# Kernel tuning notes

Hardware: AMD Instinct MI355X
Metric: run time of the kernel (lower is better)

## Reference

```python
import jax, jax.numpy as jnp
import numpy as np

DIM = 768
NUM_HEADS = 12
HEAD_DIM = 64  # attn_head_dim override
ALL_HEAD_DIM = NUM_HEADS * HEAD_DIM  # 768
SCALE = HEAD_DIM ** -0.5


def setup_inputs() -> dict:
    key = jax.random.key(0)
    ks = jax.random.split(key, 6)
    B, N = 8, 1024
    x = jax.random.normal(ks[0], (B, N, DIM), dtype=jnp.float32)
    w_qkv = jax.random.normal(ks[1], (3 * ALL_HEAD_DIM, DIM), dtype=jnp.float32) * (DIM ** -0.5)
    q_bias = jnp.zeros((ALL_HEAD_DIM,), dtype=jnp.float32)
    v_bias = jnp.zeros((ALL_HEAD_DIM,), dtype=jnp.float32)
    w_proj = jax.random.normal(ks[2], (DIM, ALL_HEAD_DIM), dtype=jnp.float32) * (ALL_HEAD_DIM ** -0.5)
    b_proj = jnp.zeros((DIM,), dtype=jnp.float32)
    return {"x": x, "w_qkv": w_qkv, "q_bias": q_bias, "v_bias": v_bias,
            "w_proj": w_proj, "b_proj": b_proj}


def reference(x, w_qkv, q_bias, v_bias, w_proj, b_proj):
    B, N, C = x.shape
    # qkv bias: [q_bias, zeros (k has no bias), v_bias]
    qkv_bias = jnp.concatenate([q_bias, jnp.zeros_like(v_bias), v_bias])
    qkv = x @ w_qkv.T + qkv_bias                      # [B, N, 3*ALL_HEAD_DIM]
    qkv = qkv.reshape(B, N, 3, NUM_HEADS, HEAD_DIM).transpose(2, 0, 3, 1, 4)
    q, k, v = qkv[0], qkv[1], qkv[2]                  # each [B, H, N, D]
    attn = jnp.einsum('bhqd,bhkd->bhqk', q * SCALE, k)
    attn = jax.nn.softmax(attn, axis=-1)
    out = jnp.einsum('bhqk,bhkd->bhqd', attn, v)      # [B, H, N, D]
    out = out.transpose(0, 2, 1, 3).reshape(B, N, ALL_HEAD_DIM)
    out = out @ w_proj.T + b_proj                     # [B, N, C]
    return out
```

## Files before the change

kernel.cpp:

```cpp
#include <hip/hip_runtime.h>
#include <hip/hip_bf16.h>

typedef unsigned short u16;
typedef unsigned int u32;
typedef __attribute__((ext_vector_type(4))) float f32x4;
typedef __attribute__((ext_vector_type(16))) float f32x16;
typedef __attribute__((ext_vector_type(8))) short bf16x8;

__device__ inline u16 f2bf(float f) {
    union { float f; u32 u; } v; v.f = f;
    u32 r = v.u + 0x7fff + ((v.u >> 16) & 1);
    return (u16)(r >> 16);
}

__device__ inline f32x4 mfma16(bf16x8 a, bf16x8 b, f32x4 c) {
    return __builtin_amdgcn_mfma_f32_16x16x32_bf16(a, b, c, 0, 0, 0);
}
__device__ inline f32x16 mfma32(bf16x8 a, bf16x8 b, f32x16 c) {
    return __builtin_amdgcn_mfma_f32_32x32x16_bf16(a, b, c, 0, 0, 0);
}
__device__ inline u32 cvtpk(float lo, float hi) {
    u32 r;
    asm("v_cvt_pk_bf16_f32 %0, %1, %2" : "=v"(r) : "v"(lo), "v"(hi));
    return r;
}
__device__ inline float exp2v(float x) {
    float r;
    asm("v_exp_f32 %0, %1" : "=v"(r) : "v"(x));
    return r;
}

__device__ inline void gload_lds16(const void* g, const void* l) {
    __builtin_amdgcn_global_load_lds(
        (const __attribute__((address_space(1))) void*)g,
        (__attribute__((address_space(3))) void*)l, 16, 0, 0);
}

#define QSCALE 0.18033688f

__global__ void cvt_kernel(const float* __restrict__ in, u16* __restrict__ out, int n8) {
    int i = blockIdx.x * 256 + threadIdx.x;
    if (i >= n8) return;
    const float4* p = (const float4*)in;
    float4 a = p[2 * i], b = p[2 * i + 1];
    bf16x8 v;
    v[0] = (short)f2bf(a.x); v[1] = (short)f2bf(a.y);
    v[2] = (short)f2bf(a.z); v[3] = (short)f2bf(a.w);
    v[4] = (short)f2bf(b.x); v[5] = (short)f2bf(b.y);
    v[6] = (short)f2bf(b.z); v[7] = (short)f2bf(b.w);
    ((bf16x8*)out)[i] = v;
}

template <int EPI>
__global__ __launch_bounds__(256) void gemm_bt(
    const u16* __restrict__ A, const u16* __restrict__ B,
    int M, int N, int K,
    u16* __restrict__ qw, u16* __restrict__ kw, u16* __restrict__ vw,
    const float* __restrict__ qb, const float* __restrict__ vb,
    float* __restrict__ outp, const float* __restrict__ bproj)
{
    __shared__ __align__(16) u16 smem[16384];
    u16* lA0 = smem;
    u16* lA1 = smem + 4096;
    u16* lB0 = smem + 8192;
    u16* lB1 = smem + 12288;

    const int tid = threadIdx.x;
    const int lane = tid & 63;
    const int wv = tid >> 6;
    const int nbn = N >> 7;
    const int nwg = gridDim.x;
    const int wg = (blockIdx.x & 7) * (nwg >> 3) + (blockIdx.x >> 3);
    const int bm = wg / nbn, bn = wg % nbn;
    const int row0 = bm << 7, col0 = bn << 7;

    const int c0 = tid, c1 = tid + 256;
    const int ldsOff0 = (wv * 64) * 8;
    const int ldsOff1 = (256 + wv * 64) * 8;

    f32x4 acc[4][4];
#pragma unroll
    for (int i = 0; i < 4; i++)
#pragma unroll
        for (int j = 0; j < 4; j++) acc[i][j] = (f32x4){0.f, 0.f, 0.f, 0.f};

    const int nT = K >> 5;

    auto stage = [&](u16* bufA, u16* bufB, int t) {
        const int k0 = t << 5;
        gload_lds16(&A[(size_t)(row0 + (c0 >> 2)) * K + k0 + (c0 & 3) * 8], bufA + ldsOff0);
        gload_lds16(&A[(size_t)(row0 + (c1 >> 2)) * K + k0 + (c1 & 3) * 8], bufA + ldsOff1);
        gload_lds16(&B[(size_t)(col0 + (c0 >> 2)) * K + k0 + (c0 & 3) * 8], bufB + ldsOff0);
        gload_lds16(&B[(size_t)(col0 + (c1 >> 2)) * K + k0 + (c1 & 3) * 8], bufB + ldsOff1);
    };

    const int wr = (wv >> 1) << 6;
    const int wc = (wv & 1) << 6;

    stage(lA0, lB0, 0);
    __syncthreads();
    for (int t = 0; t < nT; ++t) {
        const u16* As = ((t & 1) ? lA1 : lA0) + (wr + (lane & 15)) * 32 + ((lane >> 4) * 8);
        const u16* Bs = ((t & 1) ? lB1 : lB0) + (wc + (lane & 15)) * 32 + ((lane >> 4) * 8);
        if (t + 1 < nT)
            stage((t & 1) ? lA0 : lA1, (t & 1) ? lB0 : lB1, t + 1);
        bf16x8 af[4], bfr[4];
#pragma unroll
        for (int i = 0; i < 4; i++) af[i] = *(const bf16x8*)(As + i * 16 * 32);
#pragma unroll
        for (int i = 0; i < 4; i++) bfr[i] = *(const bf16x8*)(Bs + i * 16 * 32);
#pragma unroll
        for (int i = 0; i < 4; i++)
#pragma unroll
            for (int j = 0; j < 4; j++)
                acc[i][j] = mfma16(af[i], bfr[j], acc[i][j]);
        __syncthreads();
    }

    if (EPI == 0) {
        const int part = col0 / 768;
        const int colr0 = col0 - part * 768;
        const int h0 = colr0 >> 6;
        const int bb = row0 >> 10;
        const int n0 = row0 & 1023;

        if (part < 2) {
#pragma unroll
            for (int nj = 0; nj < 4; ++nj) {
                const int col = wc + nj * 16 + (lane & 15);
                const float bias = (part == 0) ? qb[colr0 + col] : 0.f;
                const float sc = (part == 0) ? QSCALE : 1.f;
#pragma unroll
                for (int mi = 0; mi < 4; ++mi) {
#pragma unroll
                    for (int j = 0; j < 4; ++j) {
                        const int row = wr + mi * 16 + ((lane >> 4) << 2) + j;
                        smem[row * 128 + ((((col >> 3) ^ (row & 7)) << 3) | (col & 7))] =
                            f2bf((acc[mi][nj][j] + bias) * sc);
                    }
                }
            }
        } else {
#pragma unroll
            for (int nj = 0; nj < 4; ++nj) {
                const int col = wc + nj * 16 + (lane & 15);
                const float bias = vb[colr0 + col];
#pragma unroll
                for (int mi = 0; mi < 4; ++mi) {
                    const int row = wr + mi * 16 + ((lane >> 4) << 2);
                    ushort4 pk;
                    pk.x = f2bf(acc[mi][nj][0] + bias);
                    pk.y = f2bf(acc[mi][nj][1] + bias);
                    pk.z = f2bf(acc[mi][nj][2] + bias);
                    pk.w = f2bf(acc[mi][nj][3] + bias);
                    *(ushort4*)&smem[col * 128 +
                        ((((row >> 3) ^ (col & 7)) << 3) | (row & 7))] = pk;
                }
            }
        }
        __syncthreads();

        if (part == 0) {
#pragma unroll
            for (int p = 0; p < 8; ++p) {
                const int c = p * 256 + tid;
                const int h = c >> 10, ri = (c >> 3) & 127, j = c & 7;
                bf16x8 v = *(const bf16x8*)&smem[ri * 128 + (((h * 8 + j) ^ (ri & 7)) << 3)];
                *(bf16x8*)&qw[((size_t)(((bb * 12 + h0 + h) << 10) + n0 + ri)) * 64 + j * 8] = v;
            }
        } else if (part == 1) {
#pragma unroll
            for (int p = 0; p < 8; ++p) {
                const int c = p * 256 + tid;
                const int h = c >> 10, t2 = (c >> 8) & 3, j = (c >> 5) & 7, r = c & 31;
                const int ri = t2 * 32 + r;
                bf16x8 v = *(const bf16x8*)&smem[ri * 128 + (((h * 8 + j) ^ (ri & 7)) << 3)];
                *(bf16x8*)&kw[((size_t)(bb * 12 + h0 + h) << 16) +
                              (((n0 >> 5) + t2) << 11) + (j << 8) + (r << 3)] = v;
            }
        } else {
#pragma unroll
            for (int p = 0; p < 8; ++p) {
                const int c = p * 256 + tid;
                const int h = c >> 10, w = c & 1023;
                const int t2 = w >> 8, f = (w >> 6) & 3, ln = w & 63;
                const int d = ((f >> 1) << 5) + (ln & 31);
                const int rb = t2 * 32 + ((f & 1) << 4) + ((ln >> 5) << 3);
                const int ct = h * 64 + d;
                bf16x8 v = *(const bf16x8*)&smem[ct * 128 + (((rb >> 3) ^ (ct & 7)) << 3)];
                *(bf16x8*)&vw[((size_t)(bb * 12 + h0 + h) << 16) +
                              (((n0 >> 5) + t2) << 11) + (f << 9) + (ln << 3)] = v;
            }
        }
    } else {
#pragma unroll
        for (int nj = 0; nj < 4; ++nj) {
            const int col = col0 + wc + nj * 16 + (lane & 15);
            const float bias = bproj[col];
#pragma unroll
            for (int mi = 0; mi < 4; ++mi) {
#pragma unroll
                for (int j = 0; j < 4; ++j) {
                    const int row = row0 + wr + mi * 16 + ((lane >> 4) << 2) + j;
                    outp[(size_t)row * N + col] = acc[mi][nj][j] + bias;
                }
            }
        }
    }
}

__global__ __launch_bounds__(256, 3) void attn_fwd(
    const u16* __restrict__ Q, const u16* __restrict__ KF,
    const u16* __restrict__ VF, u16* __restrict__ O)
{
    __shared__ __align__(16) u16 tlds[4][32 * 68];
    const int tid = threadIdx.x, lane = tid & 63, wv = tid >> 6;
    const int l31 = lane & 31, hi = lane >> 5;
    const int bh = blockIdx.x % 96;
    const int qbk = blockIdx.x / 96;
    const int q0 = qbk * 128 + wv * 32;
    const size_t base = (size_t)bh << 16;
    const u16* Qp = Q + base;
    const u16* Kp = KF + base;
    const u16* Vp = VF + base;

    bf16x8 qf0, qf1, qf2, qf3;
    {
        const u16* qrow = &Qp[(q0 + l31) * 64 + hi * 8];
        qf0 = *(const bf16x8*)(qrow);
        qf1 = *(const bf16x8*)(qrow + 16);
        qf2 = *(const bf16x8*)(qrow + 32);
        qf3 = *(const bf16x8*)(qrow + 48);
    }

    f32x16 ot0, ot1;
#pragma unroll
    for (int i = 0; i < 16; ++i) { ot0[i] = 0.f; ot1[i] = 0.f; }
    float m = -1e30f, l = 0.f;

    auto loadK = [&](int t2048, bf16x8& f0, bf16x8& f1, bf16x8& f2, bf16x8& f3) {
        const u16* kr = &Kp[t2048 + hi * 256 + l31 * 8];
        f0 = *(const bf16x8*)(kr);
        f1 = *(const bf16x8*)(kr + 512);
        f2 = *(const bf16x8*)(kr + 1024);
        f3 = *(const bf16x8*)(kr + 1536);
    };

    auto body = [&](int t2048, bf16x8 k0, bf16x8 k1, bf16x8 k2, bf16x8 k3) {
        f32x16 s;
#pragma unroll
        for (int i = 0; i < 16; ++i) s[i] = 0.f;
        __builtin_amdgcn_s_setprio(1);
        s = mfma32(k0, qf0, s);
        s = mfma32(k1, qf1, s);
        s = mfma32(k2, qf2, s);
        s = mfma32(k3, qf3, s);
        __builtin_amdgcn_s_setprio(0);
        const u16* vrow = &Vp[t2048 + lane * 8];
        bf16x8 vf00 = *(const bf16x8*)(vrow);
        bf16x8 vf01 = *(const bf16x8*)(vrow + 512);
        bf16x8 vf10 = *(const bf16x8*)(vrow + 1024);
        bf16x8 vf11 = *(const bf16x8*)(vrow + 1536);
        float t0 = fmaxf(fmaxf(s[0], s[1]), fmaxf(s[2], s[3]));
        float t1 = fmaxf(fmaxf(s[4], s[5]), fmaxf(s[6], s[7]));
        float t2 = fmaxf(fmaxf(s[8], s[9]), fmaxf(s[10], s[11]));
        float t3 = fmaxf(fmaxf(s[12], s[13]), fmaxf(s[14], s[15]));
        float tmax = fmaxf(fmaxf(t0, t1), fmaxf(t2, t3));
        tmax = fmaxf(tmax, __shfl_xor(tmax, 32));
        if (!__all(tmax - m <= 8.f)) {
            const float nm = fmaxf(m, tmax);
            const float cr = exp2v(m - nm);
#pragma unroll
            for (int i = 0; i < 16; ++i) { ot0[i] *= cr; ot1[i] *= cr; }
            l *= cr; m = nm;
        }
#pragma unroll
        for (int i = 0; i < 16; ++i) { float p = exp2v(s[i] - m); s[i] = p; l += p; }
        u32 w0 = cvtpk(s[0],  s[1]),  w1 = cvtpk(s[2],  s[3]);
        u32 w2 = cvtpk(s[4],  s[5]),  w3 = cvtpk(s[6],  s[7]);
        u32 w4 = cvtpk(s[8],  s[9]),  w5 = cvtpk(s[10], s[11]);
        u32 w6 = cvtpk(s[12], s[13]), w7 = cvtpk(s[14], s[15]);
        asm("v_permlane32_swap_b32 %0, %1" : "+v"(w0), "+v"(w2));
        asm("v_permlane32_swap_b32 %0, %1" : "+v"(w1), "+v"(w3));
        asm("v_permlane32_swap_b32 %0, %1" : "+v"(w4), "+v"(w6));
        asm("v_permlane32_swap_b32 %0, %1" : "+v"(w5), "+v"(w7));
        union { u32 u[4]; bf16x8 v; } pb0, pb1;
        pb0.u[0] = w0; pb0.u[1] = w1; pb0.u[2] = w2; pb0.u[3] = w3;
        pb1.u[0] = w4; pb1.u[1] = w5; pb1.u[2] = w6; pb1.u[3] = w7;
        __builtin_amdgcn_s_setprio(1);
        ot0 = mfma32(vf00, pb0.v, ot0);
        ot0 = mfma32(vf01, pb1.v, ot0);
        ot1 = mfma32(vf10, pb0.v, ot1);
        ot1 = mfma32(vf11, pb1.v, ot1);
        __builtin_amdgcn_s_setprio(0);
    };

    bf16x8 ka0, ka1, ka2, ka3, kb0, kb1, kb2, kb3;
    loadK(0, ka0, ka1, ka2, ka3);
    for (int kt = 0; kt < 32; kt += 2) {
        loadK((kt + 1) << 11, kb0, kb1, kb2, kb3);
        body(kt << 11, ka0, ka1, ka2, ka3);
        if (kt + 2 < 32) loadK((kt + 2) << 11, ka0, ka1, ka2, ka3);
        body((kt + 1) << 11, kb0, kb1, kb2, kb3);
    }

    const float lt = l + __shfl_xor(l, 32);
    const float inv = 1.f / lt;
    u16* tw = &tlds[wv][0];
    u32* tw32 = (u32*)tw;
#pragma unroll
    for (int i = 0; i < 8; ++i) {
        const int dl = 2 * (i & 1) + 8 * (i >> 1) + 4 * hi;
        tw32[(l31 * 68 + dl) >> 1]      = cvtpk(ot0[2 * i] * inv, ot0[2 * i + 1] * inv);
        tw32[(l31 * 68 + dl + 32) >> 1] = cvtpk(ot1[2 * i] * inv, ot1[2 * i + 1] * inv);
    }
    __syncthreads();
    const int b = bh / 12, h = bh - b * 12;
    const size_t obase = ((size_t)(b << 10) + q0) * 768 + h * 64 + (lane & 7) * 8;
#pragma unroll
    for (int it = 0; it < 4; ++it) {
        const int r = it * 8 + (lane >> 3);
        bf16x8 v = *(const bf16x8*)&tw[r * 68 + (lane & 7) * 8];
        *(bf16x8*)&O[obase + (size_t)r * 768] = v;
    }
}

extern "C" void kernel_launch(void* const* d_in, const int* in_sizes, int n_in,
                              void* d_out, int out_size, void* d_ws, size_t ws_size,
                              hipStream_t stream) {
    const float* x      = (const float*)d_in[0];
    const float* w_qkv  = (const float*)d_in[1];
    const float* q_bias = (const float*)d_in[2];
    const float* v_bias = (const float*)d_in[3];
    const float* w_proj = (const float*)d_in[4];
    const float* b_proj = (const float*)d_in[5];
    float* out = (float*)d_out;

    char* ws = (char*)d_ws;
    u16* xb     = (u16*)(ws);
    u16* wqkvb  = (u16*)(ws + 12582912);
    u16* wprojb = (u16*)(ws + 16121856);
    u16* qw     = (u16*)(ws + 17301504);
    u16* kw     = (u16*)(ws + 29884416);
    u16* vt     = (u16*)(ws + 42467328);
    u16* ob     = (u16*)(ws + 55050240);

    cvt_kernel<<<786432 / 256, 256, 0, stream>>>(x, xb, 786432);
    cvt_kernel<<<221184 / 256, 256, 0, stream>>>(w_qkv, wqkvb, 221184);
    cvt_kernel<<< 73728 / 256, 256, 0, stream>>>(w_proj, wprojb, 73728);

    gemm_bt<0><<<(8192 / 128) * (2304 / 128), 256, 0, stream>>>(
        xb, wqkvb, 8192, 2304, 768, qw, kw, vt, q_bias, v_bias, nullptr, nullptr);

    attn_fwd<<<96 * 8, 256, 0, stream>>>(qw, kw, vt, ob);

    gemm_bt<1><<<(8192 / 128) * (768 / 128), 256, 0, stream>>>(
        ob, wprojb, 8192, 768, 768, nullptr, nullptr, nullptr, nullptr, nullptr, out, b_proj);
}
```

Baseline: 123.3 us.

## Rewrite QKV GEMM with 256x256 tiles, 8 waves and triple-buffered LDS pipeline

Replaces the templated 128x128 QKV GEMM with a dedicated kernel that uses 256x256 tiles, 512 threads and a three-stage LDS ring with a swizzled layout. Each wave computes a 128x64 sub-tile, and MFMA priority hints are set around the inner products. The epilogue writes out the two 128-row halves in turn through shared memory. The aim is to raise data reuse per loaded byte and to hide global load latency, at the cost of 96KB of LDS per block, more registers, and only 288 blocks.

```diff
diff --git a/kernel.cpp b/kernel.cpp
--- a/kernel.cpp
+++ b/kernel.cpp
@@ -51,13 +51,188 @@
     ((bf16x8*)out)[i] = v;
 }
 
-template <int EPI>
-__global__ __launch_bounds__(256) void gemm_bt(
+__global__ __launch_bounds__(512, 2) void gemm_qkv(
     const u16* __restrict__ A, const u16* __restrict__ B,
-    int M, int N, int K,
     u16* __restrict__ qw, u16* __restrict__ kw, u16* __restrict__ vw,
-    const float* __restrict__ qb, const float* __restrict__ vb,
-    float* __restrict__ outp, const float* __restrict__ bproj)
+    const float* __restrict__ qb, const float* __restrict__ vb)
+{
+    __shared__ __align__(16) u16 smem[49152];
+    const int K = 768;
+    const int NT = 24;
+    const int tid = threadIdx.x;
+    const int lane = tid & 63, wv = tid >> 6;
+    const int wm = wv >> 2, wn = wv & 3;
+    const int wg = (blockIdx.x & 7) * 36 + (blockIdx.x >> 3);
+    const int bm = wg / 9, bn = wg % 9;
+    const int row0 = bm << 8, col0 = bn << 8;
+
+    const int srow = tid >> 2;
+    const int sch = (tid & 3) ^ ((srow >> 1) & 3);
+    const u16* gA = A + (size_t)(row0 + srow) * K + sch * 8;
+    const u16* gB = B + (size_t)(col0 + srow) * K + sch * 8;
+    const int ldst = wv * 512;
+
+    auto stageTile = [&](int bufi, int t) {
+        u16* base = &smem[bufi * 16384];
+        const int k0 = t << 5;
+        gload_lds16(gA + k0,                     base + ldst);
+        gload_lds16(gA + (size_t)128 * K + k0,   base + 4096 + ldst);
+        gload_lds16(gB + k0,                     base + 8192 + ldst);
+        gload_lds16(gB + (size_t)128 * K + k0,   base + 12288 + ldst);
+    };
+
+    const int arl = lane & 15, ahi = lane >> 4;
+    auto loadFrags = [&](int bufi, bf16x8 (&fa)[8], bf16x8 (&fb)[4]) {
+        const u16* bA = &smem[bufi * 16384 + wm * 4096];
+        const u16* bB = &smem[bufi * 16384 + 8192 + (wn >> 1) * 4096];
+#pragma unroll
+        for (int fi = 0; fi < 8; ++fi) {
+            const int rl = fi * 16 + arl;
+            const int chc = ahi ^ ((rl >> 1) & 3);
+            fa[fi] = *(const bf16x8*)(bA + rl * 32 + chc * 8);
+        }
+#pragma unroll
+        for (int fj = 0; fj < 4; ++fj) {
+            const int cl = ((wn & 1) << 6) + fj * 16 + arl;
+            const int chc = ahi ^ ((cl >> 1) & 3);
+            fb[fj] = *(const bf16x8*)(bB + cl * 32 + chc * 8);
+        }
+    };
+
+    f32x4 acc[8][4];
+#pragma unroll
+    for (int i = 0; i < 8; ++i)
+#pragma unroll
+        for (int j = 0; j < 4; ++j) acc[i][j] = (f32x4){0.f, 0.f, 0.f, 0.f};
+
+    auto mfmaTile = [&](bf16x8 (&fa)[8], bf16x8 (&fb)[4]) {
+#pragma unroll
+        for (int fi = 0; fi < 8; ++fi) {
+            __builtin_amdgcn_s_setprio(1);
+#pragma unroll
+            for (int fj = 0; fj < 4; ++fj)
+                acc[fi][fj] = mfma16(fa[fi], fb[fj], acc[fi][fj]);
+            __builtin_amdgcn_s_setprio(0);
+        }
+    };
+
+    bf16x8 ra[8], rb[4], sa[8], sb[4];
+
+    stageTile(0, 0); stageTile(1, 1); stageTile(2, 2);
+    asm volatile("s_waitcnt vmcnt(8)" ::: "memory");
+    __builtin_amdgcn_s_barrier();
+    loadFrags(0, ra, rb);
+    asm volatile("s_waitcnt lgkmcnt(0)" ::: "memory");
+    __builtin_amdgcn_sched_barrier(0);
+
+#pragma unroll 1
+    for (int t = 0; t < NT - 2; t += 2) {
+        asm volatile("s_waitcnt vmcnt(4)" ::: "memory");
+        __builtin_amdgcn_s_barrier();
+        stageTile(t % 3, t + 3);
+        loadFrags((t + 1) % 3, sa, sb);
+        mfmaTile(ra, rb);
+        asm volatile("s_waitcnt lgkmcnt(0)" ::: "memory");
+        __builtin_amdgcn_sched_barrier(0);
+        asm volatile("s_waitcnt vmcnt(4)" ::: "memory");
+        __builtin_amdgcn_s_barrier();
+        if (t + 4 < NT) stageTile((t + 1) % 3, t + 4);
+        loadFrags((t + 2) % 3, ra, rb);
+        mfmaTile(sa, sb);
+        asm volatile("s_waitcnt lgkmcnt(0)" ::: "memory");
+        __builtin_amdgcn_sched_barrier(0);
+    }
+    asm volatile("s_waitcnt vmcnt(0)" ::: "memory");
+    __builtin_amdgcn_s_barrier();
+    loadFrags((NT - 1) % 3, sa, sb);
+    mfmaTile(ra, rb);
+    mfmaTile(sa, sb);
+    __syncthreads();
+
+    const int part = col0 / 768;
+    const int colr0 = col0 - part * 768;
+    const int h0 = colr0 >> 6;
+
+#pragma unroll 1
+    for (int H = 0; H < 2; ++H) {
+        if (wm == H) {
+            if (part < 2) {
+#pragma unroll
+                for (int fj = 0; fj < 4; ++fj) {
+                    const int cl = wn * 64 + fj * 16 + arl;
+                    const float bias = (part == 0) ? qb[colr0 + cl] : 0.f;
+                    const float sc = (part == 0) ? QSCALE : 1.f;
+#pragma unroll
+                    for (int fi = 0; fi < 8; ++fi) {
+#pragma unroll
+                        for (int j = 0; j < 4; ++j) {
+                            const int rl = fi * 16 + (ahi << 2) + j;
+                            smem[rl * 256 + ((((cl >> 3) ^ (rl & 7)) << 3) | (cl & 7))] =
+                                f2bf((acc[fi][fj][j] + bias) * sc);
+                        }
+                    }
+                }
+            } else {
+#pragma unroll
+                for (int fj = 0; fj < 4; ++fj) {
+                    const int cl = wn * 64 + fj * 16 + arl;
+                    const float bias = vb[colr0 + cl];
+#pragma unroll
+                    for (int fi = 0; fi < 8; ++fi) {
+                        const int rl0 = fi * 16 + (ahi << 2);
+                        ushort4 pk;
+                        pk.x = f2bf(acc[fi][fj][0] + bias);
+                        pk.y = f2bf(acc[fi][fj][1] + bias);
+                        pk.z = f2bf(acc[fi][fj][2] + bias);
+                        pk.w = f2bf(acc[fi][fj][3] + bias);
+                        *(ushort4*)&smem[cl * 128 +
+                            ((((rl0 >> 3) ^ (cl & 7)) << 3) | (rl0 & 7))] = pk;
+                    }
+                }
+            }
+        }
+        __syncthreads();
+        const int bbH = (row0 + H * 128) >> 10;
+        const int n0H = (row0 + H * 128) & 1023;
+        if (part == 0) {
+#pragma unroll
+            for (int p = 0; p < 8; ++p) {
+                const int c = p * 512 + tid;
+                const int h = c >> 10, ri = (c >> 3) & 127, j = c & 7;
+                bf16x8 v = *(const bf16x8*)&smem[ri * 256 + ((((h << 3) + j) ^ (ri & 7)) << 3)];
+                *(bf16x8*)&qw[((size_t)(((bbH * 12 + h0 + h) << 10) + n0H + ri)) * 64 + j * 8] = v;
+            }
+        } else if (part == 1) {
+#pragma unroll
+            for (int p = 0; p < 8; ++p) {
+                const int c = p * 512 + tid;
+                const int h = c >> 10, t2 = (c >> 8) & 3, j = (c >> 5) & 7, r = c & 31;
+                const int ri = t2 * 32 + r;
+                bf16x8 v = *(const bf16x8*)&smem[ri * 256 + ((((h << 3) + j) ^ (ri & 7)) << 3)];
+                *(bf16x8*)&kw[((size_t)(bbH * 12 + h0 + h) << 16) +
+                              (((n0H >> 5) + t2) << 11) + (j << 8) + (r << 3)] = v;
+            }
+        } else {
+#pragma unroll
+            for (int p = 0; p < 8; ++p) {
+                const int c = p * 512 + tid;
+                const int h = c >> 10, w = c & 1023;
+                const int t2 = w >> 8, f = (w >> 6) & 3, ln = w & 63;
+                const int d = ((f >> 1) << 5) + (ln & 31);
+                const int rb_ = t2 * 32 + ((f & 1) << 4) + ((ln >> 5) << 3);
+                const int ct = h * 64 + d;
+                bf16x8 v = *(const bf16x8*)&smem[ct * 128 + (((rb_ >> 3) ^ (ct & 7)) << 3)];
+                *(bf16x8*)&vw[((size_t)(bbH * 12 + h0 + h) << 16) +
+                              (((n0H >> 5) + t2) << 11) + (f << 9) + (ln << 3)] = v;
+            }
+        }
+        __syncthreads();
+    }
+}
+
+__global__ __launch_bounds__(256) void gemm_proj(
+    const u16* __restrict__ A, const u16* __restrict__ B,
+    int M, int N, int K, float* __restrict__ outp, const float* __restrict__ bproj)
 {
     __shared__ __align__(16) u16 smem[16384];
     u16* lA0 = smem;
@@ -117,93 +292,16 @@
         __syncthreads();
     }
 
-    if (EPI == 0) {
-        const int part = col0 / 768;
-        const int colr0 = col0 - part * 768;
-        const int h0 = colr0 >> 6;
-        const int bb = row0 >> 10;
-        const int n0 = row0 & 1023;
-
-        if (part < 2) {
-#pragma unroll
-            for (int nj = 0; nj < 4; ++nj) {
-                const int col = wc + nj * 16 + (lane & 15);
-                const float bias = (part == 0) ? qb[colr0 + col] : 0.f;
-                const float sc = (part == 0) ? QSCALE : 1.f;
-#pragma unroll
-                for (int mi = 0; mi < 4; ++mi) {
-#pragma unroll
-                    for (int j = 0; j < 4; ++j) {
-                        const int row = wr + mi * 16 + ((lane >> 4) << 2) + j;
-                        smem[row * 128 + ((((col >> 3) ^ (row & 7)) << 3) | (col & 7))] =
-                            f2bf((acc[mi][nj][j] + bias) * sc);
-                    }
-                }
-            }
-        } else {
-#pragma unroll
-            for (int nj = 0; nj < 4; ++nj) {
-                const int col = wc + nj * 16 + (lane & 15);
-                const float bias = vb[colr0 + col];
-#pragma unroll
-                for (int mi = 0; mi < 4; ++mi) {
-                    const int row = wr + mi * 16 + ((lane >> 4) << 2);
-                    ushort4 pk;
-                    pk.x = f2bf(acc[mi][nj][0] + bias);
-                    pk.y = f2bf(acc[mi][nj][1] + bias);
-                    pk.z = f2bf(acc[mi][nj][2] + bias);
-                    pk.w = f2bf(acc[mi][nj][3] + bias);
-                    *(ushort4*)&smem[col * 128 +
-                        ((((row >> 3) ^ (col & 7)) << 3) | (row & 7))] = pk;
-                }
-            }
-        }
-        __syncthreads();
-
-        if (part == 0) {
-#pragma unroll
-            for (int p = 0; p < 8; ++p) {
-                const int c = p * 256 + tid;
-                const int h = c >> 10, ri = (c >> 3) & 127, j = c & 7;
-                bf16x8 v = *(const bf16x8*)&smem[ri * 128 + (((h * 8 + j) ^ (ri & 7)) << 3)];
-                *(bf16x8*)&qw[((size_t)(((bb * 12 + h0 + h) << 10) + n0 + ri)) * 64 + j * 8] = v;
-            }
-        } else if (part == 1) {
-#pragma unroll
-            for (int p = 0; p < 8; ++p) {
-                const int c = p * 256 + tid;
-                const int h = c >> 10, t2 = (c >> 8) & 3, j = (c >> 5) & 7, r = c & 31;
-                const int ri = t2 * 32 + r;
-                bf16x8 v = *(const bf16x8*)&smem[ri * 128 + (((h * 8 + j) ^ (ri & 7)) << 3)];
-                *(bf16x8*)&kw[((size_t)(bb * 12 + h0 + h) << 16) +
-                              (((n0 >> 5) + t2) << 11) + (j << 8) + (r << 3)] = v;
-            }
-        } else {
-#pragma unroll
-            for (int p = 0; p < 8; ++p) {
-                const int c = p * 256 + tid;
-                const int h = c >> 10, w = c & 1023;
-                const int t2 = w >> 8, f = (w >> 6) & 3, ln = w & 63;
-                const int d = ((f >> 1) << 5) + (ln & 31);
-                const int rb = t2 * 32 + ((f & 1) << 4) + ((ln >> 5) << 3);
-                const int ct = h * 64 + d;
-                bf16x8 v = *(const bf16x8*)&smem[ct * 128 + (((rb >> 3) ^ (ct & 7)) << 3)];
-                *(bf16x8*)&vw[((size_t)(bb * 12 + h0 + h) << 16) +
-                              (((n0 >> 5) + t2) << 11) + (f << 9) + (ln << 3)] = v;
-            }
-        }
-    } else {
-#pragma unroll
-        for (int nj = 0; nj < 4; ++nj) {
-            const int col = col0 + wc + nj * 16 + (lane & 15);
-            const float bias = bproj[col];
-#pragma unroll
-            for (int mi = 0; mi < 4; ++mi) {
-#pragma unroll
-                for (int j = 0; j < 4; ++j) {
-                    const int row = row0 + wr + mi * 16 + ((lane >> 4) << 2) + j;
-                    outp[(size_t)row * N + col] = acc[mi][nj][j] + bias;
-                }
+#pragma unroll
+    for (int nj = 0; nj < 4; ++nj) {
+        const int col = col0 + wc + nj * 16 + (lane & 15);
+        const float bias = bproj[col];
+#pragma unroll
+        for (int mi = 0; mi < 4; ++mi) {
+#pragma unroll
+            for (int j = 0; j < 4; ++j) {
+                const int row = row0 + wr + mi * 16 + ((lane >> 4) << 2) + j;
+                outp[(size_t)row * N + col] = acc[mi][nj][j] + bias;
             }
         }
     }
@@ -349,11 +447,10 @@
     cvt_kernel<<<221184 / 256, 256, 0, stream>>>(w_qkv, wqkvb, 221184);
     cvt_kernel<<< 73728 / 256, 256, 0, stream>>>(w_proj, wprojb, 73728);
 
-    gemm_bt<0><<<(8192 / 128) * (2304 / 128), 256, 0, stream>>>(
-        xb, wqkvb, 8192, 2304, 768, qw, kw, vt, q_bias, v_bias, nullptr, nullptr);
+    gemm_qkv<<<288, 512, 0, stream>>>(xb, wqkvb, qw, kw, vt, q_bias, v_bias);
 
     attn_fwd<<<96 * 8, 256, 0, stream>>>(qw, kw, vt, ob);
 
-    gemm_bt<1><<<(8192 / 128) * (768 / 128), 256, 0, stream>>>(
-        ob, wprojb, 8192, 768, 768, nullptr, nullptr, nullptr, nullptr, nullptr, out, b_proj);
-}
+    gemm_proj<<<(8192 / 128) * (768 / 128), 256, 0, stream>>>(
+        ob, wprojb, 8192, 768, 768, out, b_proj);
+}
```

Result: slower. 167.8 us (+36.1%).

## Triple-buffer GEMM LDS tiles with swizzled layout and explicit waitcnt pipelining

Applied to the files above, without the earlier changes.

Rewrites the GEMM main loop to use three LDS stages, so global-to-LDS loads run two tiles ahead. It uses explicit vmcnt/lgkmcnt waits and raw barriers instead of __syncthreads. It also XOR-swizzles the LDS tile layout to cut bank conflicts on fragment reads, and raises MFMA priority with s_setprio. The cost is more LDS per block (48KB), which may reduce occupancy, and K is hardcoded to 768.

```diff
diff --git a/kernel.cpp b/kernel.cpp
--- a/kernel.cpp
+++ b/kernel.cpp
@@ -52,70 +52,100 @@
 }
 
 template <int EPI>
-__global__ __launch_bounds__(256) void gemm_bt(
+__global__ __launch_bounds__(256) void gemm_bt3(
     const u16* __restrict__ A, const u16* __restrict__ B,
-    int M, int N, int K,
+    int nbn,
     u16* __restrict__ qw, u16* __restrict__ kw, u16* __restrict__ vw,
     const float* __restrict__ qb, const float* __restrict__ vb,
     float* __restrict__ outp, const float* __restrict__ bproj)
 {
-    __shared__ __align__(16) u16 smem[16384];
-    u16* lA0 = smem;
-    u16* lA1 = smem + 4096;
-    u16* lB0 = smem + 8192;
-    u16* lB1 = smem + 12288;
-
+    __shared__ __align__(16) u16 smem[24576];
+    const int K = 768;
+    const int NT = 24;
     const int tid = threadIdx.x;
-    const int lane = tid & 63;
-    const int wv = tid >> 6;
-    const int nbn = N >> 7;
+    const int lane = tid & 63, wv = tid >> 6;
     const int nwg = gridDim.x;
     const int wg = (blockIdx.x & 7) * (nwg >> 3) + (blockIdx.x >> 3);
     const int bm = wg / nbn, bn = wg % nbn;
     const int row0 = bm << 7, col0 = bn << 7;
 
-    const int c0 = tid, c1 = tid + 256;
-    const int ldsOff0 = (wv * 64) * 8;
-    const int ldsOff1 = (256 + wv * 64) * 8;
-
-    f32x4 acc[4][4];
-#pragma unroll
-    for (int i = 0; i < 4; i++)
-#pragma unroll
-        for (int j = 0; j < 4; j++) acc[i][j] = (f32x4){0.f, 0.f, 0.f, 0.f};
-
-    const int nT = K >> 5;
-
-    auto stage = [&](u16* bufA, u16* bufB, int t) {
+    const int srow = tid >> 2;
+    const int sch = (tid & 3) ^ ((srow >> 1) & 3);
+    const u16* gA = A + (size_t)(row0 + srow) * K + sch * 8;
+    const u16* gB = B + (size_t)(col0 + srow) * K + sch * 8;
+    const int ldst = wv * 512;
+
+    auto stageTile = [&](int bufi, int t) {
+        u16* base = &smem[bufi * 8192];
         const int k0 = t << 5;
-        gload_lds16(&A[(size_t)(row0 + (c0 >> 2)) * K + k0 + (c0 & 3) * 8], bufA + ldsOff0);
-        gload_lds16(&A[(size_t)(row0 + (c1 >> 2)) * K + k0 + (c1 & 3) * 8], bufA + ldsOff1);
-        gload_lds16(&B[(size_t)(col0 + (c0 >> 2)) * K + k0 + (c0 & 3) * 8], bufB + ldsOff0);
-        gload_lds16(&B[(size_t)(col0 + (c1 >> 2)) * K + k0 + (c1 & 3) * 8], bufB + ldsOff1);
+        gload_lds16(gA + k0,                   base + ldst);
+        gload_lds16(gA + (size_t)64 * K + k0,  base + 2048 + ldst);
+        gload_lds16(gB + k0,                   base + 4096 + ldst);
+        gload_lds16(gB + (size_t)64 * K + k0,  base + 4096 + 2048 + ldst);
     };
 
     const int wr = (wv >> 1) << 6;
     const int wc = (wv & 1) << 6;
-
-    stage(lA0, lB0, 0);
+    const int arl = lane & 15, ahi = lane >> 4;
+    bf16x8 fa[4], fb[4];
+    auto loadFrags = [&](int bufi) {
+        const u16* bA = &smem[bufi * 8192];
+        const u16* bB = &smem[bufi * 8192 + 4096];
+#pragma unroll
+        for (int fi = 0; fi < 4; ++fi) {
+            const int rl = wr + fi * 16 + arl;
+            fa[fi] = *(const bf16x8*)(bA + rl * 32 + ((ahi ^ ((rl >> 1) & 3)) << 3));
+        }
+#pragma unroll
+        for (int fj = 0; fj < 4; ++fj) {
+            const int cl = wc + fj * 16 + arl;
+            fb[fj] = *(const bf16x8*)(bB + cl * 32 + ((ahi ^ ((cl >> 1) & 3)) << 3));
+        }
+    };
+
+    f32x4 acc[4][4];
+#pragma unroll
+    for (int i = 0; i < 4; i++)
+#pragma unroll
+        for (int j = 0; j < 4; j++) acc[i][j] = (f32x4){0.f, 0.f, 0.f, 0.f};
+
+    auto mfmaTile = [&]() {
+        __builtin_amdgcn_s_setprio(1);
+#pragma unroll
+        for (int i = 0; i < 4; i++)
+#pragma unroll
+            for (int j = 0; j < 4; j++)
+                acc[i][j] = mfma16(fa[i], fb[j], acc[i][j]);
+        __builtin_amdgcn_s_setprio(0);
+    };
+
+    stageTile(0, 0); stageTile(1, 1); stageTile(2, 2);
+
+#pragma unroll 1
+    for (int t = 0; t < NT - 2; ++t) {
+        asm volatile("s_waitcnt vmcnt(8)" ::: "memory");
+        __builtin_amdgcn_s_barrier();
+        loadFrags(t % 3);
+        asm volatile("s_waitcnt lgkmcnt(0)" ::: "memory");
+        __builtin_amdgcn_sched_barrier(0);
+        __builtin_amdgcn_s_barrier();
+        if (t < NT - 3) stageTile(t % 3, t + 3);
+        __builtin_amdgcn_sched_barrier(0);
+        mfmaTile();
+    }
+    asm volatile("s_waitcnt vmcnt(4)" ::: "memory");
+    __builtin_amdgcn_s_barrier();
+    loadFrags(22 % 3);
+    asm volatile("s_waitcnt lgkmcnt(0)" ::: "memory");
+    __builtin_amdgcn_sched_barrier(0);
+    mfmaTile();
+    asm volatile("s_waitcnt vmcnt(0)" ::: "memory");
+    __builtin_amdgcn_s_barrier();
+    loadFrags(23 % 3);
+    asm volatile("s_waitcnt lgkmcnt(0)" ::: "memory");
+    __builtin_amdgcn_sched_barrier(0);
+    mfmaTile();
     __syncthreads();
-    for (int t = 0; t < nT; ++t) {
-        const u16* As = ((t & 1) ? lA1 : lA0) + (wr + (lane & 15)) * 32 + ((lane >> 4) * 8);
-        const u16* Bs = ((t & 1) ? lB1 : lB0) + (wc + (lane & 15)) * 32 + ((lane >> 4) * 8);
-        if (t + 1 < nT)
-            stage((t & 1) ? lA0 : lA1, (t & 1) ? lB0 : lB1, t + 1);
-        bf16x8 af[4], bfr[4];
-#pragma unroll
-        for (int i = 0; i < 4; i++) af[i] = *(const bf16x8*)(As + i * 16 * 32);
-#pragma unroll
-        for (int i = 0; i < 4; i++) bfr[i] = *(const bf16x8*)(Bs + i * 16 * 32);
-#pragma unroll
-        for (int i = 0; i < 4; i++)
-#pragma unroll
-            for (int j = 0; j < 4; j++)
-                acc[i][j] = mfma16(af[i], bfr[j], acc[i][j]);
-        __syncthreads();
-    }
 
     if (EPI == 0) {
         const int part = col0 / 768;
@@ -127,14 +157,14 @@
         if (part < 2) {
 #pragma unroll
             for (int nj = 0; nj < 4; ++nj) {
-                const int col = wc + nj * 16 + (lane & 15);
+                const int col = wc + nj * 16 + arl;
                 const float bias = (part == 0) ? qb[colr0 + col] : 0.f;
                 const float sc = (part == 0) ? QSCALE : 1.f;
 #pragma unroll
                 for (int mi = 0; mi < 4; ++mi) {
 #pragma unroll
                     for (int j = 0; j < 4; ++j) {
-                        const int row = wr + mi * 16 + ((lane >> 4) << 2) + j;
+                        const int row = wr + mi * 16 + (ahi << 2) + j;
                         smem[row * 128 + ((((col >> 3) ^ (row & 7)) << 3) | (col & 7))] =
                             f2bf((acc[mi][nj][j] + bias) * sc);
                     }
@@ -143,11 +173,11 @@
         } else {
 #pragma unroll
             for (int nj = 0; nj < 4; ++nj) {
-                const int col = wc + nj * 16 + (lane & 15);
+                const int col = wc + nj * 16 + arl;
                 const float bias = vb[colr0 + col];
 #pragma unroll
                 for (int mi = 0; mi < 4; ++mi) {
-                    const int row = wr + mi * 16 + ((lane >> 4) << 2);
+                    const int row = wr + mi * 16 + (ahi << 2);
                     ushort4 pk;
                     pk.x = f2bf(acc[mi][nj][0] + bias);
                     pk.y = f2bf(acc[mi][nj][1] + bias);
@@ -165,7 +195,7 @@
             for (int p = 0; p < 8; ++p) {
                 const int c = p * 256 + tid;
                 const int h = c >> 10, ri = (c >> 3) & 127, j = c & 7;
-                bf16x8 v = *(const bf16x8*)&smem[ri * 128 + (((h * 8 + j) ^ (ri & 7)) << 3)];
+                bf16x8 v = *(const bf16x8*)&smem[ri * 128 + ((((h << 3) + j) ^ (ri & 7)) << 3)];
                 *(bf16x8*)&qw[((size_t)(((bb * 12 + h0 + h) << 10) + n0 + ri)) * 64 + j * 8] = v;
             }
         } else if (part == 1) {
@@ -174,7 +204,7 @@
                 const int c = p * 256 + tid;
                 const int h = c >> 10, t2 = (c >> 8) & 3, j = (c >> 5) & 7, r = c & 31;
                 const int ri = t2 * 32 + r;
-                bf16x8 v = *(const bf16x8*)&smem[ri * 128 + (((h * 8 + j) ^ (ri & 7)) << 3)];
+                bf16x8 v = *(const bf16x8*)&smem[ri * 128 + ((((h << 3) + j) ^ (ri & 7)) << 3)];
                 *(bf16x8*)&kw[((size_t)(bb * 12 + h0 + h) << 16) +
                               (((n0 >> 5) + t2) << 11) + (j << 8) + (r << 3)] = v;
             }
@@ -185,23 +215,24 @@
                 const int h = c >> 10, w = c & 1023;
                 const int t2 = w >> 8, f = (w >> 6) & 3, ln = w & 63;
                 const int d = ((f >> 1) << 5) + (ln & 31);
-                const int rb = t2 * 32 + ((f & 1) << 4) + ((ln >> 5) << 3);
+                const int rb_ = t2 * 32 + ((f & 1) << 4) + ((ln >> 5) << 3);
                 const int ct = h * 64 + d;
-                bf16x8 v = *(const bf16x8*)&smem[ct * 128 + (((rb >> 3) ^ (ct & 7)) << 3)];
+                bf16x8 v = *(const bf16x8*)&smem[ct * 128 + (((rb_ >> 3) ^ (ct & 7)) << 3)];
                 *(bf16x8*)&vw[((size_t)(bb * 12 + h0 + h) << 16) +
                               (((n0 >> 5) + t2) << 11) + (f << 9) + (ln << 3)] = v;
             }
         }
     } else {
+        const int N = nbn << 7;
 #pragma unroll
         for (int nj = 0; nj < 4; ++nj) {
-            const int col = col0 + wc + nj * 16 + (lane & 15);
+            const int col = col0 + wc + nj * 16 + arl;
             const float bias = bproj[col];
 #pragma unroll
             for (int mi = 0; mi < 4; ++mi) {
 #pragma unroll
                 for (int j = 0; j < 4; ++j) {
-                    const int row = row0 + wr + mi * 16 + ((lane >> 4) << 2) + j;
+                    const int row = row0 + wr + mi * 16 + (ahi << 2) + j;
                     outp[(size_t)row * N + col] = acc[mi][nj][j] + bias;
                 }
             }
@@ -349,11 +380,11 @@
     cvt_kernel<<<221184 / 256, 256, 0, stream>>>(w_qkv, wqkvb, 221184);
     cvt_kernel<<< 73728 / 256, 256, 0, stream>>>(w_proj, wprojb, 73728);
 
-    gemm_bt<0><<<(8192 / 128) * (2304 / 128), 256, 0, stream>>>(
-        xb, wqkvb, 8192, 2304, 768, qw, kw, vt, q_bias, v_bias, nullptr, nullptr);
+    gemm_bt3<0><<<(8192 / 128) * (2304 / 128), 256, 0, stream>>>(
+        xb, wqkvb, 2304 / 128, qw, kw, vt, q_bias, v_bias, nullptr, nullptr);
 
     attn_fwd<<<96 * 8, 256, 0, stream>>>(qw, kw, vt, ob);
 
-    gemm_bt<1><<<(8192 / 128) * (768 / 128), 256, 0, stream>>>(
-        ob, wprojb, 8192, 768, 768, nullptr, nullptr, nullptr, nullptr, nullptr, out, b_proj);
-}
+    gemm_bt3<1><<<(8192 / 128) * (768 / 128), 256, 0, stream>>>(
+        ob, wprojb, 768 / 128, nullptr, nullptr, nullptr, nullptr, nullptr, out, b_proj);
+}
```

Result: faster. 114.7 us (-7.0%).
